# Performance work log

Measured on AMD Instinct MI355X. Metric: run time of the kernel, lower is better.

The kernel has to match this reference:

```python
import jax, jax.numpy as jnp
import numpy as np

B, I, C, J, D, H, W = 16, 32, 8, 10, 16, 6, 6
NUM_ROUTING = 3
EPS = 1e-07


def setup_inputs() -> dict:
    key = jax.random.key(0)
    u_hat = jax.random.normal(key, (B, I, C, J, D, H, W), dtype=jnp.float32)
    # torch module fills bias with 0.1, shape (out_capsules, out_channels, 1, 1)
    bias = jnp.full((J, D, 1, 1), 0.1, dtype=jnp.float32)
    return {"u_hat": u_hat, "bias": bias, "num_routing": NUM_ROUTING}


def _squash(s):
    # Faithful to the source: L1 norm over ALL non-batch dims (not per-capsule L2).
    n1 = jnp.sum(jnp.abs(s), axis=(1, 2, 3, 4), keepdims=True)  # [B,1,1,1,1]
    n1_sq = n1 * n1
    return (n1_sq / (1.0 + n1_sq)) * (s / (n1 + EPS))


def reference(u_hat, bias, num_routing):
    # u_hat: [B,I,C,J,D,H,W]; bias: [J,D,1,1]
    b_ij = jnp.zeros((I, J), dtype=u_hat.dtype)
    v_j = None
    for _ in range(num_routing):
        c_ij = jax.nn.softmax(b_ij, axis=1)  # [I,J]
        # s_j[b,j,d,h,w] = sum_{i,c} c[i,j] * u_hat[b,i,c,j,d,h,w]  (c broadcast over in_channels)
        s_j = jnp.einsum('ij,bicjdhw->bjdhw', c_ij, u_hat) + bias
        v_j = _squash(s_j)  # [B,J,D,H,W]
        # agreement[i,j] = sum over b,c,d,h,w of u_hat * v_j (broadcast over i,c)
        agreement = jnp.einsum('bicjdhw,bjdhw->ij', u_hat, v_j)
        b_ij = b_ij + jax.lax.stop_gradient(agreement)  # torch uses .data (detached)
    return v_j
```

## Files before the change

### kernel.cpp

```cpp
#include <hip/hip_runtime.h>


#define NB   16
#define NI   32
#define NC   8
#define NJ   10
#define ND   16
#define NHW  36
#define NDHW 576
#define NTOT (NB * NJ * NDHW)
#define EPSV 1e-7f
#define TPB  576
#define NBLK 160

static __device__ __forceinline__ double wave_sum(double v) {
    #pragma unroll
    for (int off = 32; off > 0; off >>= 1) v += __shfl_down(v, off);
    return v;
}

static __device__ __forceinline__ void n1_reduce(float sv, double* slot,
                                                 double* nred ) {
    int tid = threadIdx.x;
    double a = wave_sum((double)fabsf(sv));
    if ((tid & 63) == 0) nred[tid >> 6] = a;
    __syncthreads();
    if (tid == 0) {
        double t = nred[0];
        #pragma unroll
        for (int w = 1; w < 9; ++w) t += nred[w];
        *slot = t;
    }
}

static __device__ __forceinline__ void g_reduce(const float* Uv, float sv,
                                                double* gslot,
                                                double (*gred)[32] ) {
    int tid = threadIdx.x, w = tid >> 6, lane = tid & 63;
    #pragma unroll
    for (int i = 0; i < NI; ++i) {
        double p = wave_sum((double)Uv[i] * (double)sv);
        if (lane == 0) gred[w][i] = p;
    }
    __syncthreads();
    if (tid < NI) {
        double t = gred[0][tid];
        #pragma unroll
        for (int w2 = 1; w2 < 9; ++w2) t += gred[w2][tid];
        gslot[tid] = t;
    }
}

static __device__ __forceinline__ void grid_barrier(unsigned* cnt,
                                                    unsigned* rel, int tid) {
    __syncthreads();
    if (tid == 0) {
        __threadfence();
        unsigned old = __hip_atomic_fetch_add(cnt, 1u, __ATOMIC_ACQ_REL,
                                              __HIP_MEMORY_SCOPE_AGENT);
        if (old == NBLK - 1) {
            __hip_atomic_store(rel, 1u, __ATOMIC_RELEASE,
                               __HIP_MEMORY_SCOPE_AGENT);
        } else {
            while (__hip_atomic_load(rel, __ATOMIC_ACQUIRE,
                                     __HIP_MEMORY_SCOPE_AGENT) == 0u)
                __builtin_amdgcn_s_sleep(8);
        }
    }
    __syncthreads();
}

static __device__ __forceinline__ void fold_c(
    int R, int j, int tid,
    const double* __restrict__ n1p, const double* __restrict__ Gp,
    double (*sc_sh)[NB], float* bij_sh, float* c_sh)
{
    if (tid < R * NB) {
        int rr = tid / NB, bb = tid - rr * NB;
        double n1 = 0.0;
        #pragma unroll
        for (int jj = 0; jj < NJ; ++jj) n1 += n1p[rr * (NB * NJ) + bb * NJ + jj];
        double nsq = n1 * n1;
        sc_sh[rr][bb] = (nsq / (1.0 + nsq)) / (n1 + (double)EPSV);
    }
    __syncthreads();
    if (tid < NI * NJ) {
        int i = tid / NJ, jj = tid - i * NJ;
        double a = 0.0;
        for (int rr = 0; rr < R; ++rr)
            #pragma unroll
            for (int bb = 0; bb < NB; ++bb)
                a += sc_sh[rr][bb] *
                     Gp[(size_t)(rr * NB + bb) * NJ * NI + (size_t)jj * NI + i];
        bij_sh[tid] = (float)a;
    }
    __syncthreads();
    if (tid < NI) {
        float m = -1e30f;
        #pragma unroll
        for (int jj = 0; jj < NJ; ++jj) m = fmaxf(m, bij_sh[tid * NJ + jj]);
        float sum = 0.f;
        #pragma unroll
        for (int jj = 0; jj < NJ; ++jj) sum += expf(bij_sh[tid * NJ + jj] - m);
        c_sh[tid] = expf(bij_sh[tid * NJ + j] - m) / sum;
    }
    __syncthreads();
}

__global__ __launch_bounds__(TPB) void mega_kernel(
    const float4* __restrict__ uh4, const float* __restrict__ bias,
    double* __restrict__ n1p, double* __restrict__ Gp,
    unsigned* __restrict__ bar, float* __restrict__ out)
{
    __shared__ float4  Utile4[NI * 144];
    __shared__ double  nred[9];
    __shared__ double  gred[9][32];
    __shared__ double  sc_sh[2][NB];
    __shared__ float   bij_sh[NI * NJ];
    __shared__ float   c_sh[NI];

    const int blk = blockIdx.x;
    const int b = blk / NJ, j = blk - b * NJ;
    const int tid = threadIdx.x;

    #pragma unroll
    for (int g = 0; g < 8; ++g) {
        int lin = g * TPB + tid;
        int i = lin / 144, f4 = lin - i * 144;
        const float4* p = uh4 + ((size_t)(b * NI + i) * NC) * 1440 + j * 144 + f4;
        float4 acc = make_float4(0.f, 0.f, 0.f, 0.f);
        #pragma unroll
        for (int c = 0; c < NC; ++c) {
            float4 v = p[(size_t)c * 1440];
            acc.x += v.x; acc.y += v.y; acc.z += v.z; acc.w += v.w;
        }
        Utile4[lin] = acc;
    }
    __syncthreads();

    const float* Utile = (const float*)Utile4;
    float Uv[NI];
    #pragma unroll
    for (int i = 0; i < NI; ++i) Uv[i] = Utile[i * NDHW + tid];
    const float bias_v = bias[j * ND + tid / NHW];

    float sv = bias_v;
    #pragma unroll
    for (int i = 0; i < NI; ++i) sv += 0.1f * Uv[i];
    n1_reduce(sv, &n1p[blk], nred);
    g_reduce(Uv, sv, &Gp[(size_t)blk * NI], gred);
    grid_barrier(&bar[0], &bar[3], tid);

    fold_c(1, j, tid, n1p, Gp, sc_sh, bij_sh, c_sh);
    sv = bias_v;
    #pragma unroll
    for (int i = 0; i < NI; ++i) sv += c_sh[i] * Uv[i];
    n1_reduce(sv, &n1p[NB * NJ + blk], nred);
    g_reduce(Uv, sv, &Gp[(size_t)(NB * NJ + blk) * NI], gred);
    grid_barrier(&bar[1], &bar[4], tid);

    fold_c(2, j, tid, n1p, Gp, sc_sh, bij_sh, c_sh);
    sv = bias_v;
    #pragma unroll
    for (int i = 0; i < NI; ++i) sv += c_sh[i] * Uv[i];
    n1_reduce(sv, &n1p[2 * NB * NJ + blk], nred);
    grid_barrier(&bar[2], &bar[5], tid);

    double n1 = 0.0;
    #pragma unroll
    for (int jj = 0; jj < NJ; ++jj) n1 += n1p[2 * NB * NJ + b * NJ + jj];
    float n1f = (float)n1;
    float nsq = n1f * n1f;
    out[blk * NDHW + tid] = (nsq / (1.f + nsq)) * (sv / (n1f + EPSV));
}

extern "C" void kernel_launch(void* const* d_in, const int* in_sizes, int n_in,
                              void* d_out, int out_size, void* d_ws, size_t ws_size,
                              hipStream_t stream)
{
    const float* u_hat = (const float*)d_in[0];
    const float* bias  = (const float*)d_in[1];

    unsigned* bar = (unsigned*)d_ws;
    double*   n1p = (double*)((char*)d_ws + 32);
    double*   Gp  = n1p + 3 * NB * NJ;
    float*    out = (float*)d_out;

    hipMemsetAsync(bar, 0, 6 * sizeof(unsigned), stream);
    mega_kernel<<<NBLK, TPB, 0, stream>>>(
        (const float4*)u_hat, bias, n1p, Gp, bar, out);
}
```

Before: 205.5 us.

## Split routing across 480 blocks with global C-reduced buffer and atomic partials

Raises the persistent kernel from 160 to 480 blocks of 256 threads. Every block first reduces u_hat over C into a global buffer, then a grid barrier follows, and each block loads a 192-element chunk of one (b,j) tile into padded LDS. Per-batch L1 norms and the G agreement partials are now accumulated with double atomics instead of per-block slots that were summed afterwards, and the routing loop runs as a single loop over rounds. The aim is more parallelism for the memory-bound C reduction and a lighter fold step. The cost is an extra grid barrier, a round trip of the reduced tensor through global memory, atomic contention, and four grid barriers across 480 co-resident blocks.

Result: slower. 382.4 us (+86.1%).

```diff
diff --git a/kernel.cpp b/kernel.cpp
--- a/kernel.cpp
+++ b/kernel.cpp
@@ -8,47 +8,16 @@
 #define ND   16
 #define NHW  36
 #define NDHW 576
-#define NTOT (NB * NJ * NDHW)
 #define EPSV 1e-7f
-#define TPB  576
-#define NBLK 160
+#define TPB  256
+#define NBLK 480
+#define CHUNK 192
+#define LSTR 193
 
-static __device__ __forceinline__ double wave_sum(double v) {
+static __device__ __forceinline__ double wave_sum64(double v) {
     #pragma unroll
     for (int off = 32; off > 0; off >>= 1) v += __shfl_down(v, off);
     return v;
-}
-
-static __device__ __forceinline__ void n1_reduce(float sv, double* slot,
-                                                 double* nred ) {
-    int tid = threadIdx.x;
-    double a = wave_sum((double)fabsf(sv));
-    if ((tid & 63) == 0) nred[tid >> 6] = a;
-    __syncthreads();
-    if (tid == 0) {
-        double t = nred[0];
-        #pragma unroll
-        for (int w = 1; w < 9; ++w) t += nred[w];
-        *slot = t;
-    }
-}
-
-static __device__ __forceinline__ void g_reduce(const float* Uv, float sv,
-                                                double* gslot,
-                                                double (*gred)[32] ) {
-    int tid = threadIdx.x, w = tid >> 6, lane = tid & 63;
-    #pragma unroll
-    for (int i = 0; i < NI; ++i) {
-        double p = wave_sum((double)Uv[i] * (double)sv);
-        if (lane == 0) gred[w][i] = p;
-    }
-    __syncthreads();
-    if (tid < NI) {
-        double t = gred[0][tid];
-        #pragma unroll
-        for (int w2 = 1; w2 < 9; ++w2) t += gred[w2][tid];
-        gslot[tid] = t;
-    }
 }
 
 static __device__ __forceinline__ void grid_barrier(unsigned* cnt,
@@ -70,108 +39,136 @@
     __syncthreads();
 }
 
-static __device__ __forceinline__ void fold_c(
-    int R, int j, int tid,
-    const double* __restrict__ n1p, const double* __restrict__ Gp,
-    double (*sc_sh)[NB], float* bij_sh, float* c_sh)
-{
-    if (tid < R * NB) {
-        int rr = tid / NB, bb = tid - rr * NB;
-        double n1 = 0.0;
-        #pragma unroll
-        for (int jj = 0; jj < NJ; ++jj) n1 += n1p[rr * (NB * NJ) + bb * NJ + jj];
-        double nsq = n1 * n1;
-        sc_sh[rr][bb] = (nsq / (1.0 + nsq)) / (n1 + (double)EPSV);
-    }
-    __syncthreads();
-    if (tid < NI * NJ) {
-        int i = tid / NJ, jj = tid - i * NJ;
-        double a = 0.0;
-        for (int rr = 0; rr < R; ++rr)
-            #pragma unroll
-            for (int bb = 0; bb < NB; ++bb)
-                a += sc_sh[rr][bb] *
-                     Gp[(size_t)(rr * NB + bb) * NJ * NI + (size_t)jj * NI + i];
-        bij_sh[tid] = (float)a;
-    }
-    __syncthreads();
-    if (tid < NI) {
-        float m = -1e30f;
-        #pragma unroll
-        for (int jj = 0; jj < NJ; ++jj) m = fmaxf(m, bij_sh[tid * NJ + jj]);
-        float sum = 0.f;
-        #pragma unroll
-        for (int jj = 0; jj < NJ; ++jj) sum += expf(bij_sh[tid * NJ + jj] - m);
-        c_sh[tid] = expf(bij_sh[tid * NJ + j] - m) / sum;
-    }
-    __syncthreads();
-}
-
 __global__ __launch_bounds__(TPB) void mega_kernel(
     const float4* __restrict__ uh4, const float* __restrict__ bias,
-    double* __restrict__ n1p, double* __restrict__ Gp,
-    unsigned* __restrict__ bar, float* __restrict__ out)
+    float4* __restrict__ U2f4, double* __restrict__ n1p,
+    double* __restrict__ Gp, unsigned* __restrict__ bar,
+    float* __restrict__ out)
 {
-    __shared__ float4  Utile4[NI * 144];
-    __shared__ double  nred[9];
-    __shared__ double  gred[9][32];
-    __shared__ double  sc_sh[2][NB];
-    __shared__ float   bij_sh[NI * NJ];
-    __shared__ float   c_sh[NI];
+    __shared__ float  Utile[NI * LSTR];
+    __shared__ float  s_sh[CHUNK];
+    __shared__ double sc_sh[2][NB];
+    __shared__ float  bij_sh[NI * NJ];
+    __shared__ float  c_sh[NI];
 
     const int blk = blockIdx.x;
-    const int b = blk / NJ, j = blk - b * NJ;
+    const int tile  = blk / 3;
+    const int chunk = blk - tile * 3;
+    const int b = tile / NJ, j = tile - b * NJ;
     const int tid = threadIdx.x;
 
     #pragma unroll
-    for (int g = 0; g < 8; ++g) {
-        int lin = g * TPB + tid;
-        int i = lin / 144, f4 = lin - i * 144;
-        const float4* p = uh4 + ((size_t)(b * NI + i) * NC) * 1440 + j * 144 + f4;
+    for (int it = 0; it < 6; ++it) {
+        int t  = it * (NBLK * TPB) + blk * TPB + tid;
+        int f4 = t % 144;
+        int i  = (t / 144) % NI;
+        int jj = (t / (144 * NI)) % NJ;
+        int bb = t / (144 * NI * NJ);
+        const float4* p = uh4 + ((size_t)(bb * NI + i) * NC) * 1440 + jj * 144 + f4;
         float4 acc = make_float4(0.f, 0.f, 0.f, 0.f);
         #pragma unroll
         for (int c = 0; c < NC; ++c) {
             float4 v = p[(size_t)c * 1440];
             acc.x += v.x; acc.y += v.y; acc.z += v.z; acc.w += v.w;
         }
-        Utile4[lin] = acc;
+        U2f4[t] = acc;
+    }
+    grid_barrier(&bar[0], &bar[4], tid);
+
+    {
+        const float* U2 = (const float*)U2f4;
+        const float* src = U2 + (size_t)tile * NI * NDHW + chunk * CHUNK;
+        if (tid < CHUNK) {
+            #pragma unroll 8
+            for (int i = 0; i < NI; ++i)
+                Utile[i * LSTR + tid] = src[i * NDHW + tid];
+        }
     }
     __syncthreads();
 
-    const float* Utile = (const float*)Utile4;
-    float Uv[NI];
-    #pragma unroll
-    for (int i = 0; i < NI; ++i) Uv[i] = Utile[i * NDHW + tid];
-    const float bias_v = bias[j * ND + tid / NHW];
+    const float bias_v = (tid < CHUNK)
+        ? bias[j * ND + (chunk * CHUNK + tid) / NHW] : 0.f;
 
-    float sv = bias_v;
-    #pragma unroll
-    for (int i = 0; i < NI; ++i) sv += 0.1f * Uv[i];
-    n1_reduce(sv, &n1p[blk], nred);
-    g_reduce(Uv, sv, &Gp[(size_t)blk * NI], gred);
-    grid_barrier(&bar[0], &bar[3], tid);
+    for (int r = 0; r < 3; ++r) {
+        if (r == 0) {
+            if (tid < NI) c_sh[tid] = 0.1f;
+            __syncthreads();
+        } else {
+            if (tid < r * NB) {
+                int rr = tid / NB, bb = tid - rr * NB;
+                double n1v = n1p[rr * NB + bb];
+                double nsq = n1v * n1v;
+                sc_sh[rr][bb] = (nsq / (1.0 + nsq)) / (n1v + (double)EPSV);
+            }
+            __syncthreads();
+            for (int t = tid; t < NI * NJ; t += TPB) {
+                int i = t / NJ, jj = t - i * NJ;
+                double a = 0.0;
+                for (int rr = 0; rr < r; ++rr)
+                    #pragma unroll
+                    for (int bb = 0; bb < NB; ++bb)
+                        a += sc_sh[rr][bb] *
+                             Gp[(size_t)rr * (NB * NJ * NI) +
+                                (size_t)(bb * NJ + jj) * NI + i];
+                bij_sh[t] = (float)a;
+            }
+            __syncthreads();
+            if (tid < NI) {
+                float m = -1e30f;
+                #pragma unroll
+                for (int jj = 0; jj < NJ; ++jj)
+                    m = fmaxf(m, bij_sh[tid * NJ + jj]);
+                float sum = 0.f;
+                #pragma unroll
+                for (int jj = 0; jj < NJ; ++jj)
+                    sum += expf(bij_sh[tid * NJ + jj] - m);
+                c_sh[tid] = expf(bij_sh[tid * NJ + j] - m) / sum;
+            }
+            __syncthreads();
+        }
 
-    fold_c(1, j, tid, n1p, Gp, sc_sh, bij_sh, c_sh);
-    sv = bias_v;
-    #pragma unroll
-    for (int i = 0; i < NI; ++i) sv += c_sh[i] * Uv[i];
-    n1_reduce(sv, &n1p[NB * NJ + blk], nred);
-    g_reduce(Uv, sv, &Gp[(size_t)(NB * NJ + blk) * NI], gred);
-    grid_barrier(&bar[1], &bar[4], tid);
+        if (tid < CHUNK) {
+            float sv = bias_v;
+            #pragma unroll
+            for (int i = 0; i < NI; ++i)
+                sv += c_sh[i] * Utile[i * LSTR + tid];
+            s_sh[tid] = sv;
+        }
+        __syncthreads();
 
-    fold_c(2, j, tid, n1p, Gp, sc_sh, bij_sh, c_sh);
-    sv = bias_v;
-    #pragma unroll
-    for (int i = 0; i < NI; ++i) sv += c_sh[i] * Uv[i];
-    n1_reduce(sv, &n1p[2 * NB * NJ + blk], nred);
-    grid_barrier(&bar[2], &bar[5], tid);
+        if (tid < 64) {
+            double a = (double)fabsf(s_sh[tid]) +
+                       (double)fabsf(s_sh[tid + 64]) +
+                       (double)fabsf(s_sh[tid + 128]);
+            a = wave_sum64(a);
+            if (tid == 0)
+                atomicAdd(&n1p[r * NB + b], a);
+        }
 
-    double n1 = 0.0;
-    #pragma unroll
-    for (int jj = 0; jj < NJ; ++jj) n1 += n1p[2 * NB * NJ + b * NJ + jj];
-    float n1f = (float)n1;
-    float nsq = n1f * n1f;
-    out[blk * NDHW + tid] = (nsq / (1.f + nsq)) * (sv / (n1f + EPSV));
+        if (r < 2) {
+            int i = tid >> 3, k = tid & 7;
+            const float* Ui = &Utile[i * LSTR + k * 24];
+            const float* sk = &s_sh[k * 24];
+            double p = 0.0;
+            #pragma unroll
+            for (int m = 0; m < 24; ++m)
+                p += (double)Ui[m] * (double)sk[m];
+            p += __shfl_down(p, 4);
+            p += __shfl_down(p, 2);
+            p += __shfl_down(p, 1);
+            if (k == 0)
+                atomicAdd(&Gp[(size_t)r * (NB * NJ * NI) +
+                              (size_t)(b * NJ + j) * NI + i], p);
+        }
+        grid_barrier(&bar[1 + r], &bar[5 + r], tid);
+    }
+
+    if (tid < CHUNK) {
+        float n1f = (float)n1p[2 * NB + b];
+        float nsq = n1f * n1f;
+        out[(size_t)tile * NDHW + chunk * CHUNK + tid] =
+            (nsq / (1.f + nsq)) * (s_sh[tid] / (n1f + EPSV));
+    }
 }
 
 extern "C" void kernel_launch(void* const* d_in, const int* in_sizes, int n_in,
@@ -182,11 +179,12 @@
     const float* bias  = (const float*)d_in[1];
 
     unsigned* bar = (unsigned*)d_ws;
-    double*   n1p = (double*)((char*)d_ws + 32);
-    double*   Gp  = n1p + 3 * NB * NJ;
+    double*   n1p = (double*)((char*)d_ws + 64);
+    double*   Gp  = (double*)((char*)d_ws + 448);
+    float*    U2  = (float*)((char*)d_ws + 131072);
     float*    out = (float*)d_out;
 
-    hipMemsetAsync(bar, 0, 6 * sizeof(unsigned), stream);
+    hipMemsetAsync(d_ws, 0, 448 + 2 * NB * NJ * NI * sizeof(double), stream);
     mega_kernel<<<NBLK, TPB, 0, stream>>>(
-        (const float4*)u_hat, bias, n1p, Gp, bar, out);
+        (const float4*)u_hat, bias, (float4*)U2, n1p, Gp, bar, out);
 }
```
